# Performance work log

Hardware: AMD Instinct MI355X
Metric: run time of the kernel (lower is better)

The kernel has to match this reference:

```python
import jax, jax.numpy as jnp
import numpy as np

B, N, CPTS = 16, 4096, 64
M, K, RADIUS = 1024, 32, 0.2
MLP = [64, 64, 128]
EPS = 1e-5  # torch BatchNorm2d default


def setup_inputs() -> dict:
    key = jax.random.key(0)
    ks = jax.random.split(key, 2 + len(MLP))
    inp = {
        "xyz": jax.random.uniform(ks[0], (B, N, 3), dtype=jnp.float32),
        "points": jax.random.normal(ks[1], (B, N, CPTS), dtype=jnp.float32),
    }
    cin = 3 + CPTS
    for i, cout in enumerate(MLP):
        inp[f"W{i}"] = jax.random.normal(ks[2 + i], (cout, cin), dtype=jnp.float32) / np.sqrt(cin)
        inp[f"g{i}"] = jnp.ones((cout,), jnp.float32)
        inp[f"b{i}"] = jnp.zeros((cout,), jnp.float32)
        cin = cout
    return inp


def fps(xyz, m):
    # Farthest point sampling, deterministic start at index 0. Returns (B, m) int32.
    b, n, _ = xyz.shape

    def step(carry, _):
        min_d, far = carry
        cent = jnp.take_along_axis(xyz, far[:, None, None], axis=1)  # (B,1,3)
        d = jnp.sum((xyz - cent) ** 2, axis=-1)                      # (B,N)
        min_d = jnp.minimum(min_d, d)
        return (min_d, jnp.argmax(min_d, axis=-1).astype(jnp.int32)), far

    init = (jnp.full((b, n), 1e10, xyz.dtype), jnp.zeros((b,), jnp.int32))
    _, inds = jax.lax.scan(step, init, None, length=m)
    return inds.T  # (B, m)


def ball_query(xyz, new_xyz, radius, k):
    # Euclidean distances (B,M,N); indices within radius, first-k, pad with first valid.
    d2 = (jnp.sum(new_xyz ** 2, -1)[:, :, None] + jnp.sum(xyz ** 2, -1)[:, None, :]
          - 2.0 * jnp.einsum('bmc,bnc->bmn', new_xyz, xyz))
    dists = jnp.sqrt(jnp.maximum(d2, 0.0))
    n = xyz.shape[1]
    idx = jnp.where(dists > radius, n, jnp.arange(n, dtype=jnp.int32)[None, None, :])
    idx = jnp.sort(idx, axis=-1)[:, :, :k]          # first k in-radius indices (N-padded)
    first = idx[:, :, :1]                           # centroid itself (dist 0) always valid
    return jnp.where(idx == n, first, idx)          # (B, M, k)


def reference(xyz, points, W0, g0, b0, W1, g1, b1, W2, g2, b2):
    bidx = jnp.arange(B)[:, None]
    fps_inds = fps(xyz, M)                          # (B, M)
    new_xyz = xyz[bidx, fps_inds]                   # (B, M, 3)
    g_inds = ball_query(xyz, new_xyz, RADIUS, K)    # (B, M, K)
    bidx2 = jnp.arange(B)[:, None, None]
    grouped_xyz = xyz[bidx2, g_inds] - new_xyz[:, :, None, :]   # (B,M,K,3) local coords
    grouped_pts = points[bidx2, g_inds]                          # (B,M,K,C)
    feats = jnp.concatenate([grouped_xyz, grouped_pts], axis=-1)  # (B,M,K,3+C)

    # 1x1 Conv2d (no bias) + BatchNorm2d (training-mode batch stats) + ReLU
    for Wi, gi, bi in ((W0, g0, b0), (W1, g1, b1), (W2, g2, b2)):
        h = jnp.einsum('bmkc,oc->bmko', feats, Wi)
        mean = h.mean(axis=(0, 1, 2))
        var = h.var(axis=(0, 1, 2))
        feats = jax.nn.relu(gi * (h - mean) * jax.lax.rsqrt(var + EPS) + bi)

    new_points = feats.max(axis=2)                  # max-pool over K -> (B, M, 128)
    return new_xyz, new_points, g_inds
```

## Files before the change

### kernel.cpp

```cpp
#include <hip/hip_runtime.h>
#include <hip/hip_bf16.h>
#include <cstdint>

#define B_ 16
#define N_ 4096
#define CPTS_ 64
#define M_ 1024
#define K_ 32
#define MF_TOT 2097152

using ushort8 = __attribute__((ext_vector_type(8))) unsigned short;

static __device__ __forceinline__ unsigned f2bf(float x){
  unsigned u = __float_as_uint(x);
  return (u + 0x7fffu + ((u >> 16) & 1u)) >> 16;
}
static __device__ __forceinline__ float bf2f(unsigned short u){
  return __uint_as_float(((unsigned)u) << 16);
}

#define DPPMAX(v, ctrl)                                                        \
  do {                                                                         \
    int _t = __builtin_amdgcn_update_dpp(0, __float_as_int(v), (ctrl), 0xf,    \
                                         0xf, true);                           \
    (v) = fmaxf((v), __int_as_float(_t));                                      \
  } while (0)

#define STEP(MD, PX, PY, PZ, C, J)                                             \
  { float dx = PX.C - cx, dy = PY.C - cy, dz = PZ.C - cz;                      \
    float d = dx * dx; d = d + dy * dy; d = d + dz * dz;                       \
    float nm = fminf(MD.C, d); MD.C = nm;                                      \
    if (nm > bv){ bv = nm; bj = (J); } }
#define STEP4(MD, PX, PY, PZ, J0)                                              \
  STEP(MD, PX, PY, PZ, x, J0)                                                  \
  STEP(MD, PX, PY, PZ, y, (J0) + 1)                                            \
  STEP(MD, PX, PY, PZ, z, (J0) + 2)                                            \
  STEP(MD, PX, PY, PZ, w, (J0) + 3)

__global__ __launch_bounds__(512, 1) void fps_kernel(const float* __restrict__ xyz,
                                                     float* __restrict__ newxyz){
#pragma clang fp contract(off)
  __shared__ float xs[N_], ys[N_], zs[N_];
  __shared__ int inds_s[M_];
  __shared__ unsigned long long sv_[2][8];
  const int b = blockIdx.x, tid = threadIdx.x;
  const int lane = tid & 63, wv = tid >> 6;
  const float* xb = xyz + (size_t)b * N_ * 3;
  for (int i = tid; i < N_ * 3; i += 512){
    float v = xb[i];
    int n = i / 3, c = i - n * 3;
    if (c == 0) xs[n] = v; else if (c == 1) ys[n] = v; else zs[n] = v;
  }
  __syncthreads();
  const float4 px0 = *reinterpret_cast<const float4*>(&xs[tid * 8 + 0]);
  const float4 px1 = *reinterpret_cast<const float4*>(&xs[tid * 8 + 4]);
  const float4 py0 = *reinterpret_cast<const float4*>(&ys[tid * 8 + 0]);
  const float4 py1 = *reinterpret_cast<const float4*>(&ys[tid * 8 + 4]);
  const float4 pz0 = *reinterpret_cast<const float4*>(&zs[tid * 8 + 0]);
  const float4 pz1 = *reinterpret_cast<const float4*>(&zs[tid * 8 + 4]);
  float4 md0 = make_float4(1e10f, 1e10f, 1e10f, 1e10f);
  float4 md1 = md0;
  int far = 0;
  float cx = xs[0], cy = ys[0], cz = zs[0];
  for (int m = 0; m < M_; ++m){
    if (tid == 0) inds_s[m] = far;
    float bv = -1.0f; int bj = 0;
    STEP4(md0, px0, py0, pz0, 0)
    STEP4(md1, px1, py1, pz1, 4)
    float wm = bv;
    DPPMAX(wm, 0x111);
    DPPMAX(wm, 0x112);
    DPPMAX(wm, 0x114);
    DPPMAX(wm, 0x118);
    DPPMAX(wm, 0x142);
    DPPMAX(wm, 0x143);
    const float wmax = __int_as_float(
        __builtin_amdgcn_readlane(__float_as_int(wm), 63));
    unsigned long long tied = __ballot(bv == wmax);
    const int winlane = (int)__builtin_ctzll(tied);
    const int sl = m & 1;
    if (lane == winlane){
      int wn = tid * 8 + bj;
      sv_[sl][wv] = ((unsigned long long)__float_as_uint(wmax) << 32)
                  | (unsigned)(4095 - wn);
    }
    __syncthreads();
    unsigned long long p0 = sv_[sl][0], p1 = sv_[sl][1], p2 = sv_[sl][2], p3 = sv_[sl][3];
    unsigned long long p4 = sv_[sl][4], p5 = sv_[sl][5], p6 = sv_[sl][6], p7 = sv_[sl][7];
    if (p1 > p0) p0 = p1;
    if (p3 > p2) p2 = p3;
    if (p5 > p4) p4 = p5;
    if (p7 > p6) p6 = p7;
    if (p2 > p0) p0 = p2;
    if (p6 > p4) p4 = p6;
    if (p4 > p0) p0 = p4;
    far = 4095 - (int)(p0 & 0xffffffffu);
    cx = xs[far]; cy = ys[far]; cz = zs[far];
  }
  __syncthreads();
  for (int t = tid; t < M_; t += 512){
    int id = inds_s[t];
    size_t o = ((size_t)b * M_ + t) * 3;
    newxyz[o] = xs[id]; newxyz[o + 1] = ys[id]; newxyz[o + 2] = zs[id];
  }
}

__global__ __launch_bounds__(256) void phi_kernel(const float* __restrict__ xyz,
                                                  const float* __restrict__ points,
                                                  const float* __restrict__ W,
                                                  float* __restrict__ phi){
  __shared__ __align__(16) float Wt[67][64];
  __shared__ __align__(16) float ft[67][128];
  const int tid = threadIdx.x, blk = blockIdx.x;
  const int p0 = blk * 128;
  for (int i = tid; i < 67 * 64; i += 256){
    int o = i / 67, c = i - o * 67;
    Wt[c][o] = W[i];
  }
  const int sl = tid >> 1, half = tid & 1;
  const int p = p0 + sl;
  const float* ps = points + (size_t)p * CPTS_ + half * 32;
  #pragma unroll
  for (int j = 0; j < 8; ++j){
    float4 v = *reinterpret_cast<const float4*>(ps + j * 4);
    int c = 3 + half * 32 + j * 4;
    ft[c][sl] = v.x; ft[c + 1][sl] = v.y; ft[c + 2][sl] = v.z; ft[c + 3][sl] = v.w;
  }
  if (half == 0){
    const float* xp = xyz + (size_t)p * 3;
    ft[0][sl] = xp[0]; ft[1][sl] = xp[1]; ft[2][sl] = xp[2];
  }
  __syncthreads();
  const int sg = tid & 31, og = tid >> 5;
  float acc[4][8];
  #pragma unroll
  for (int i = 0; i < 4; ++i)
    #pragma unroll
    for (int o = 0; o < 8; ++o) acc[i][o] = 0.0f;
  #pragma unroll 2
  for (int c = 0; c < 67; ++c){
    float4 f = *reinterpret_cast<const float4*>(&ft[c][sg * 4]);
    float4 w0 = *reinterpret_cast<const float4*>(&Wt[c][og * 8]);
    float4 w1 = *reinterpret_cast<const float4*>(&Wt[c][og * 8 + 4]);
    const float fv[4] = {f.x, f.y, f.z, f.w};
    #pragma unroll
    for (int i = 0; i < 4; ++i){
      acc[i][0] += fv[i] * w0.x; acc[i][1] += fv[i] * w0.y;
      acc[i][2] += fv[i] * w0.z; acc[i][3] += fv[i] * w0.w;
      acc[i][4] += fv[i] * w1.x; acc[i][5] += fv[i] * w1.y;
      acc[i][6] += fv[i] * w1.z; acc[i][7] += fv[i] * w1.w;
    }
  }
  #pragma unroll
  for (int i = 0; i < 4; ++i){
    float* dst = phi + (size_t)(p0 + sg * 4 + i) * 64 + og * 8;
    *reinterpret_cast<float4*>(dst)     = make_float4(acc[i][0], acc[i][1], acc[i][2], acc[i][3]);
    *reinterpret_cast<float4*>(dst + 4) = make_float4(acc[i][4], acc[i][5], acc[i][6], acc[i][7]);
  }
}

__global__ __launch_bounds__(256) void ballq_psi_kernel(const float* __restrict__ xyz,
                                                        const float* __restrict__ newxyz,
                                                        int* __restrict__ gi,
                                                        float* __restrict__ gif,
                                                        const float* __restrict__ W0,
                                                        float* __restrict__ psi){
  if (blockIdx.x >= 4096){
    const int mi = (blockIdx.x - 4096) * 256 + threadIdx.x;
    const float x = newxyz[(size_t)mi * 3];
    const float y = newxyz[(size_t)mi * 3 + 1];
    const float z = newxyz[(size_t)mi * 3 + 2];
    float* dst = psi + (size_t)mi * 64;
    #pragma unroll
    for (int o4 = 0; o4 < 16; ++o4){
      float v[4];
      #pragma unroll
      for (int e = 0; e < 4; ++e){
        int o = o4 * 4 + e;
        v[e] = fmaf(z, W0[o * 67 + 2], fmaf(y, W0[o * 67 + 1], x * W0[o * 67]));
      }
      *reinterpret_cast<float4*>(dst + o4 * 4) = make_float4(v[0], v[1], v[2], v[3]);
    }
    return;
  }
  const int gw = (blockIdx.x * 256 + threadIdx.x) >> 6;
  const int lane = threadIdx.x & 63;
  const int b = gw >> 10, m = gw & 1023;
  const float* xb = xyz + (size_t)b * N_ * 3;
  const size_t no = (size_t)b * M_ + m;
  const float cx = newxyz[no * 3], cy = newxyz[no * 3 + 1], cz = newxyz[no * 3 + 2];
  const float sm = fmaf(cz, cz, fmaf(cy, cy, cx * cx));
  int total = 0, first_idx = 0; bool havef = false;
  int*   gd = gi  + no * K_;
  float* fd = gif + no * K_;
  for (int ch = 0; ch < 64 && total < K_; ++ch){
    const int n = ch * 64 + lane;
    const float x = xb[n * 3], y = xb[n * 3 + 1], z = xb[n * 3 + 2];
    const float sn = fmaf(z, z, fmaf(y, y, x * x));
    const float dt = fmaf(z, cz, fmaf(y, cy, x * cx));
    float d2 = (sm + sn) - 2.0f * dt;
    float dist = sqrtf(fmaxf(d2, 0.0f));
    bool pred = !(dist > 0.2f);
    unsigned long long mask = __ballot(pred);
    if (!havef && mask){ havef = true; first_idx = ch * 64 + (int)__builtin_ctzll(mask); }
    if (pred){
      int rank = total + (int)__popcll(mask & ((1ull << lane) - 1ull));
      if (rank < K_){ gd[rank] = n; fd[rank] = (float)n; }
    }
    total += (int)__popcll(mask);
  }
  if (total < K_ && lane >= total && lane < K_){ gd[lane] = first_idx; fd[lane] = (float)first_idx; }
}

__global__ __launch_bounds__(256) void stats0_kernel(const float* __restrict__ phi,
                                                     const float* __restrict__ psi,
                                                     const int* __restrict__ gi,
                                                     float* __restrict__ part){
  __shared__ int gidx[128];
  __shared__ float psm[4][64];
  const int tid = threadIdx.x, blk = blockIdx.x;
  const size_t s0 = (size_t)blk * 128;
  const int b  = (int)(s0 >> 15);
  const int m0 = ((int)(s0 & 32767)) >> 5;
  if (tid < 128) gidx[tid] = gi[(size_t)b * 32768 + (size_t)m0 * K_ + tid];
  psm[tid >> 6][tid & 63] =
      psi[((size_t)b * M_ + m0 + (tid >> 6)) * 64 + (tid & 63)];
  __syncthreads();
  const int sg = tid & 31, og = tid >> 5;
  const int mi = sg >> 3;
  float sv[8], sq[8];
  #pragma unroll
  for (int o = 0; o < 8; ++o){ sv[o] = 0.f; sq[o] = 0.f; }
  #pragma unroll
  for (int i = 0; i < 4; ++i){
    const int g = gidx[sg * 4 + i];
    const float* gp = phi + ((size_t)b * N_ + g) * 64 + og * 8;
    float4 a0 = *reinterpret_cast<const float4*>(gp);
    float4 a1 = *reinterpret_cast<const float4*>(gp + 4);
    const float pv[8] = {a0.x, a0.y, a0.z, a0.w, a1.x, a1.y, a1.z, a1.w};
    #pragma unroll
    for (int o = 0; o < 8; ++o){
      float v = pv[o] - psm[mi][og * 8 + o];
      sv[o] += v; sq[o] += v * v;
    }
  }
  #pragma unroll
  for (int off = 1; off < 32; off <<= 1){
    #pragma unroll
    for (int o = 0; o < 8; ++o){
      sv[o] += __shfl_xor(sv[o], off);
      sq[o] += __shfl_xor(sq[o], off);
    }
  }
  if (sg == 0){
    #pragma unroll
    for (int o = 0; o < 8; ++o){
      int ch = og * 8 + o;
      part[(size_t)(ch * 2) * 4096 + blk]     = sv[o];
      part[(size_t)(ch * 2 + 1) * 4096 + blk] = sq[o];
    }
  }
}

template<int CIN, int COUT, int MIN_, int MOUT_>
__global__ __launch_bounds__(256) void mlp_pass(
    const float* __restrict__ phi, const float* __restrict__ psi,
    const int* __restrict__ gi,
    const unsigned short* __restrict__ hin, const float* __restrict__ bnin,
    const float* __restrict__ W,
    unsigned short* __restrict__ hout, float* __restrict__ part,
    float* __restrict__ out)
{
  constexpr int OPT = COUT / 8;
  static_assert(OPT % 4 == 0, "OPT");
  __shared__ __align__(16) float Wt[CIN][COUT];
  __shared__ __align__(16) float ft[CIN][128];
  const int tid = threadIdx.x, blk = blockIdx.x;
  const size_t s0 = (size_t)blk * 128;

  for (int i = tid; i < CIN * COUT; i += 256){
    int o = i / CIN, c = i - o * CIN;
    Wt[c][o] = W[i];
  }

  if constexpr (MIN_ == 3){
    __shared__ int gidx[128];
    __shared__ float psm[4][64];
    const int b  = (int)(s0 >> 15);
    const int m0 = ((int)(s0 & 32767)) >> 5;
    if (tid < 128) gidx[tid] = gi[(size_t)b * 32768 + (size_t)m0 * K_ + tid];
    psm[tid >> 6][tid & 63] =
        psi[((size_t)b * M_ + m0 + (tid >> 6)) * 64 + (tid & 63)];
    __syncthreads();
    const int sl = tid >> 1, half = tid & 1;
    const int g = gidx[sl];
    const int mi = sl >> 5;
    const float* gp = phi + ((size_t)b * N_ + g) * 64 + half * 32;
    #pragma unroll
    for (int j = 0; j < 8; ++j){
      float4 v = *reinterpret_cast<const float4*>(gp + j * 4);
      int c = half * 32 + j * 4;
      ft[c][sl]     = fmaxf((v.x - psm[mi][c])     * bnin[c]     + bnin[CIN + c],     0.0f);
      ft[c + 1][sl] = fmaxf((v.y - psm[mi][c + 1]) * bnin[c + 1] + bnin[CIN + c + 1], 0.0f);
      ft[c + 2][sl] = fmaxf((v.z - psm[mi][c + 2]) * bnin[c + 2] + bnin[CIN + c + 2], 0.0f);
      ft[c + 3][sl] = fmaxf((v.w - psm[mi][c + 3]) * bnin[c + 3] + bnin[CIN + c + 3], 0.0f);
    }
  } else {
    const int sl = tid >> 1, c0 = (tid & 1) * 32;
    const unsigned short* hp = hin + (s0 + sl) * CIN + c0;
    #pragma unroll
    for (int j = 0; j < 4; ++j){
      ushort8 raw = *reinterpret_cast<const ushort8*>(hp + j * 8);
      #pragma unroll
      for (int e = 0; e < 8; ++e){
        int c = c0 + j * 8 + e;
        float h = bf2f(raw[e]);
        float f = h * bnin[c] + bnin[CIN + c];
        ft[c][sl] = fmaxf(f, 0.0f);
      }
    }
  }
  __syncthreads();

  const int sg = tid & 31, og = tid >> 5;
  float acc[4][OPT];
  #pragma unroll
  for (int i = 0; i < 4; ++i)
    #pragma unroll
    for (int o = 0; o < OPT; ++o) acc[i][o] = 0.0f;

  #pragma unroll 2
  for (int c = 0; c < CIN; ++c){
    float4 f = *reinterpret_cast<const float4*>(&ft[c][sg * 4]);
    float4 w[OPT / 4];
    #pragma unroll
    for (int j = 0; j < OPT / 4; ++j)
      w[j] = *reinterpret_cast<const float4*>(&Wt[c][og * OPT + j * 4]);
    const float fv[4] = {f.x, f.y, f.z, f.w};
    #pragma unroll
    for (int i = 0; i < 4; ++i){
      #pragma unroll
      for (int j = 0; j < OPT / 4; ++j){
        acc[i][j * 4 + 0] += fv[i] * w[j].x;
        acc[i][j * 4 + 1] += fv[i] * w[j].y;
        acc[i][j * 4 + 2] += fv[i] * w[j].z;
        acc[i][j * 4 + 3] += fv[i] * w[j].w;
      }
    }
  }

  if constexpr (MOUT_ == 0){
    #pragma unroll
    for (int i = 0; i < 4; ++i){
      size_t s = s0 + sg * 4 + i;
      unsigned pk[OPT / 2];
      #pragma unroll
      for (int o = 0; o < OPT / 2; ++o)
        pk[o] = f2bf(acc[i][2 * o]) | (f2bf(acc[i][2 * o + 1]) << 16);
      uint4* dst = reinterpret_cast<uint4*>(hout + s * COUT + og * OPT);
      dst[0] = make_uint4(pk[0], pk[1], pk[2], pk[3]);
      if constexpr (OPT == 16) dst[1] = make_uint4(pk[4], pk[5], pk[6], pk[7]);
    }
  }
  {
    float sv[OPT], sq[OPT];
    #pragma unroll
    for (int o = 0; o < OPT; ++o){
      float a0 = acc[0][o], a1 = acc[1][o], a2 = acc[2][o], a3 = acc[3][o];
      sv[o] = ((a0 + a1) + a2) + a3;
      sq[o] = ((a0 * a0 + a1 * a1) + a2 * a2) + a3 * a3;
    }
    #pragma unroll
    for (int off = 1; off < 32; off <<= 1){
      #pragma unroll
      for (int o = 0; o < OPT; ++o){
        sv[o] += __shfl_xor(sv[o], off);
        sq[o] += __shfl_xor(sq[o], off);
      }
    }
    if (sg == 0){
      #pragma unroll
      for (int o = 0; o < OPT; ++o){
        int ch = og * OPT + o;
        part[(size_t)(ch * 2) * 4096 + blk]     = sv[o];
        part[(size_t)(ch * 2 + 1) * 4096 + blk] = sq[o];
      }
    }
  }
  if constexpr (MOUT_ == 4){
    float amx[OPT], amn[OPT];
    #pragma unroll
    for (int o = 0; o < OPT; ++o){
      amx[o] = fmaxf(fmaxf(acc[0][o], acc[1][o]), fmaxf(acc[2][o], acc[3][o]));
      amn[o] = fminf(fminf(acc[0][o], acc[1][o]), fminf(acc[2][o], acc[3][o]));
    }
    #pragma unroll
    for (int off = 1; off < 8; off <<= 1){
      #pragma unroll
      for (int o = 0; o < OPT; ++o){
        amx[o] = fmaxf(amx[o], __shfl_xor(amx[o], off));
        amn[o] = fminf(amn[o], __shfl_xor(amn[o], off));
      }
    }
    if ((sg & 7) == 0){
      size_t mf = (s0 >> 5) + (sg >> 3);
      float* dmx = out + mf * COUT + og * OPT;
      float* dmn = dmx + MF_TOT;
      #pragma unroll
      for (int j = 0; j < OPT / 4; ++j){
        *reinterpret_cast<float4*>(dmx + j * 4) =
            make_float4(amx[j * 4], amx[j * 4 + 1], amx[j * 4 + 2], amx[j * 4 + 3]);
        *reinterpret_cast<float4*>(dmn + j * 4) =
            make_float4(amn[j * 4], amn[j * 4 + 1], amn[j * 4 + 2], amn[j * 4 + 3]);
      }
    }
  }
}

__global__ __launch_bounds__(256) void reduce_stats(const float* __restrict__ part,
                                                    const float* __restrict__ g,
                                                    const float* __restrict__ bb,
                                                    float* __restrict__ bn, int cout){
  const int ch = blockIdx.x, tid = threadIdx.x;
  float s = 0.f, q = 0.f;
  const float* ps = part + (size_t)(ch * 2) * 4096;
  const float* pq = part + (size_t)(ch * 2 + 1) * 4096;
  for (int i = tid; i < 4096; i += 256){ s += ps[i]; q += pq[i]; }
  #pragma unroll
  for (int off = 1; off < 64; off <<= 1){ s += __shfl_xor(s, off); q += __shfl_xor(q, off); }
  __shared__ float as_[4], aq_[4];
  if ((tid & 63) == 0){ as_[tid >> 6] = s; aq_[tid >> 6] = q; }
  __syncthreads();
  if (tid == 0){
    float S = as_[0] + as_[1] + as_[2] + as_[3];
    float Q = aq_[0] + aq_[1] + aq_[2] + aq_[3];
    const float cnt = 524288.0f;
    float mean = S / cnt;
    float var  = Q / cnt - mean * mean;
    float sc = g[ch] / sqrtf(var + 1e-5f);
    bn[ch] = sc;
    bn[cout + ch] = bb[ch] - mean * sc;
  }
}

__global__ __launch_bounds__(256) void bn_minmax_finish(const float* __restrict__ mxmn,
                                                        const float* __restrict__ bn2,
                                                        float* __restrict__ out){
  const int i = blockIdx.x * 256 + threadIdx.x;
  const int ch = i & 127;
  const float a = bn2[ch], sh = bn2[128 + ch];
  const float mx = mxmn[i], mn = mxmn[MF_TOT + i];
  out[i] = fmaxf(fmaxf(mx * a + sh, mn * a + sh), 0.0f);
}

extern "C" void kernel_launch(void* const* d_in, const int* in_sizes, int n_in,
                              void* d_out, int out_size, void* d_ws, size_t ws_size,
                              hipStream_t stream){
  (void)in_sizes; (void)n_in; (void)out_size; (void)ws_size;
  const float* xyz    = (const float*)d_in[0];
  const float* points = (const float*)d_in[1];
  const float* W0 = (const float*)d_in[2];
  const float* g0 = (const float*)d_in[3];
  const float* b0 = (const float*)d_in[4];
  const float* W1 = (const float*)d_in[5];
  const float* g1 = (const float*)d_in[6];
  const float* b1 = (const float*)d_in[7];
  const float* W2 = (const float*)d_in[8];
  const float* g2 = (const float*)d_in[9];
  const float* b2 = (const float*)d_in[10];

  float* out = (float*)d_out;
  float* o_newxyz = out;
  float* o_newpts = out + (size_t)B_ * M_ * 3;
  float* o_gind   = out + (size_t)B_ * M_ * 3 + (size_t)B_ * M_ * 128;

  char* ws = (char*)d_ws;
  int*   gi   = (int*)(ws + 0);
  float* part = (float*)(ws + (2ull << 20));
  float* bn0  = (float*)(ws + (6ull << 20));
  float* bn1  = (float*)(ws + (6ull << 20) + 1024);
  float* bn2  = (float*)(ws + (6ull << 20) + 2048);
  float* phi  = (float*)(ws + (8ull << 20));
  float* psi  = (float*)(ws + (24ull << 20));
  unsigned short* h1 = (unsigned short*)(ws + (28ull << 20));
  float* mxmn = (float*)(ws + (92ull << 20));

  phi_kernel<<<512, 256, 0, stream>>>(xyz, points, W0, phi);
  fps_kernel<<<16, 512, 0, stream>>>(xyz, o_newxyz);
  ballq_psi_kernel<<<4160, 256, 0, stream>>>(xyz, o_newxyz, gi, o_gind, W0, psi);

  stats0_kernel<<<4096, 256, 0, stream>>>(phi, psi, gi, part);
  reduce_stats<<<64, 256, 0, stream>>>(part, g0, b0, bn0, 64);

  mlp_pass<64, 64, 3, 0><<<4096, 256, 0, stream>>>(phi, psi, gi,
      nullptr, bn0, W1, h1, part, nullptr);
  reduce_stats<<<64, 256, 0, stream>>>(part, g1, b1, bn1, 64);

  mlp_pass<64, 128, 1, 4><<<4096, 256, 0, stream>>>(nullptr, nullptr, nullptr,
      h1, bn1, W2, nullptr, part, mxmn);
  reduce_stats<<<128, 256, 0, stream>>>(part, g2, b2, bn2, 128);
  bn_minmax_finish<<<MF_TOT / 256, 256, 0, stream>>>(mxmn, bn2, o_newpts);
}
```

Baseline: 1.048 ms.

## Run third MLP layer on bf16 MFMA with split hi/lo precision

The 64->128 layer moves off the scalar FP32 FMA loop and onto MFMA 16x16x32 bf16 instructions. Activations and weights are each split into a bf16 high part and a bf16 residual, and three MFMAs per product recover near-FP32 accuracy. The kernel's epilogue now takes BN statistics and per-group max/min directly from the MFMA accumulator layout. The original template is specialised into a layer-1-only kernel. The cost is three MFMAs per tile and more LDS for the split operands, and accuracy is slightly below true FP32.

```diff
diff --git a/kernel.cpp b/kernel.cpp
--- a/kernel.cpp
+++ b/kernel.cpp
@@ -10,6 +10,8 @@
 #define MF_TOT 2097152
 
 using ushort8 = __attribute__((ext_vector_type(8))) unsigned short;
+using bf16x8  = __attribute__((ext_vector_type(8))) short;
+using f32x4v  = __attribute__((ext_vector_type(4))) float;
 
 static __device__ __forceinline__ unsigned f2bf(float x){
   unsigned u = __float_as_uint(x);
@@ -262,17 +264,14 @@
   }
 }
 
-template<int CIN, int COUT, int MIN_, int MOUT_>
-__global__ __launch_bounds__(256) void mlp_pass(
+template<int CIN, int COUT>
+__global__ __launch_bounds__(256) void mlp1_pass(
     const float* __restrict__ phi, const float* __restrict__ psi,
-    const int* __restrict__ gi,
-    const unsigned short* __restrict__ hin, const float* __restrict__ bnin,
+    const int* __restrict__ gi, const float* __restrict__ bnin,
     const float* __restrict__ W,
-    unsigned short* __restrict__ hout, float* __restrict__ part,
-    float* __restrict__ out)
+    unsigned short* __restrict__ hout, float* __restrict__ part)
 {
   constexpr int OPT = COUT / 8;
-  static_assert(OPT % 4 == 0, "OPT");
   __shared__ __align__(16) float Wt[CIN][COUT];
   __shared__ __align__(16) float ft[CIN][128];
   const int tid = threadIdx.x, blk = blockIdx.x;
@@ -282,8 +281,7 @@
     int o = i / CIN, c = i - o * CIN;
     Wt[c][o] = W[i];
   }
-
-  if constexpr (MIN_ == 3){
+  {
     __shared__ int gidx[128];
     __shared__ float psm[4][64];
     const int b  = (int)(s0 >> 15);
@@ -305,20 +303,6 @@
       ft[c + 2][sl] = fmaxf((v.z - psm[mi][c + 2]) * bnin[c + 2] + bnin[CIN + c + 2], 0.0f);
       ft[c + 3][sl] = fmaxf((v.w - psm[mi][c + 3]) * bnin[c + 3] + bnin[CIN + c + 3], 0.0f);
     }
-  } else {
-    const int sl = tid >> 1, c0 = (tid & 1) * 32;
-    const unsigned short* hp = hin + (s0 + sl) * CIN + c0;
-    #pragma unroll
-    for (int j = 0; j < 4; ++j){
-      ushort8 raw = *reinterpret_cast<const ushort8*>(hp + j * 8);
-      #pragma unroll
-      for (int e = 0; e < 8; ++e){
-        int c = c0 + j * 8 + e;
-        float h = bf2f(raw[e]);
-        float f = h * bnin[c] + bnin[CIN + c];
-        ft[c][sl] = fmaxf(f, 0.0f);
-      }
-    }
   }
   __syncthreads();
 
@@ -349,69 +333,156 @@
     }
   }
 
-  if constexpr (MOUT_ == 0){
-    #pragma unroll
-    for (int i = 0; i < 4; ++i){
-      size_t s = s0 + sg * 4 + i;
-      unsigned pk[OPT / 2];
+  #pragma unroll
+  for (int i = 0; i < 4; ++i){
+    size_t s = s0 + sg * 4 + i;
+    unsigned pk[OPT / 2];
+    #pragma unroll
+    for (int o = 0; o < OPT / 2; ++o)
+      pk[o] = f2bf(acc[i][2 * o]) | (f2bf(acc[i][2 * o + 1]) << 16);
+    uint4* dst = reinterpret_cast<uint4*>(hout + s * COUT + og * OPT);
+    dst[0] = make_uint4(pk[0], pk[1], pk[2], pk[3]);
+  }
+  float sv[OPT], sq[OPT];
+  #pragma unroll
+  for (int o = 0; o < OPT; ++o){
+    float a0 = acc[0][o], a1 = acc[1][o], a2 = acc[2][o], a3 = acc[3][o];
+    sv[o] = ((a0 + a1) + a2) + a3;
+    sq[o] = ((a0 * a0 + a1 * a1) + a2 * a2) + a3 * a3;
+  }
+  #pragma unroll
+  for (int off = 1; off < 32; off <<= 1){
+    #pragma unroll
+    for (int o = 0; o < OPT; ++o){
+      sv[o] += __shfl_xor(sv[o], off);
+      sq[o] += __shfl_xor(sq[o], off);
+    }
+  }
+  if (sg == 0){
+    #pragma unroll
+    for (int o = 0; o < OPT; ++o){
+      int ch = og * OPT + o;
+      part[(size_t)(ch * 2) * 4096 + blk]     = sv[o];
+      part[(size_t)(ch * 2 + 1) * 4096 + blk] = sq[o];
+    }
+  }
+}
+
+__global__ __launch_bounds__(256) void mlp2_mfma(
+    const unsigned short* __restrict__ h1, const float* __restrict__ bn1,
+    const float* __restrict__ W2, float* __restrict__ part,
+    float* __restrict__ mxmn)
+{
+  __shared__ unsigned short wsh[128 * 72], wsl[128 * 72];
+  __shared__ unsigned short fsh[128 * 72], fsl[128 * 72];
+  const int tid = threadIdx.x, blk = blockIdx.x;
+  const size_t s0 = (size_t)blk * 128;
+
+  for (int i = tid; i < 128 * 64; i += 256){
+    int o = i >> 6, c = i & 63;
+    float f = W2[i];
+    unsigned hb = f2bf(f);
+    float res = f - bf2f((unsigned short)hb);
+    wsh[o * 72 + c] = (unsigned short)hb;
+    wsl[o * 72 + c] = (unsigned short)f2bf(res);
+  }
+  {
+    const int sl = tid >> 1, c0 = (tid & 1) * 32;
+    const unsigned short* hp = h1 + (s0 + sl) * 64 + c0;
+    #pragma unroll
+    for (int j = 0; j < 4; ++j){
+      ushort8 raw = *reinterpret_cast<const ushort8*>(hp + j * 8);
+      ushort8 ph, pl;
       #pragma unroll
-      for (int o = 0; o < OPT / 2; ++o)
-        pk[o] = f2bf(acc[i][2 * o]) | (f2bf(acc[i][2 * o + 1]) << 16);
-      uint4* dst = reinterpret_cast<uint4*>(hout + s * COUT + og * OPT);
-      dst[0] = make_uint4(pk[0], pk[1], pk[2], pk[3]);
-      if constexpr (OPT == 16) dst[1] = make_uint4(pk[4], pk[5], pk[6], pk[7]);
-    }
-  }
-  {
-    float sv[OPT], sq[OPT];
-    #pragma unroll
-    for (int o = 0; o < OPT; ++o){
-      float a0 = acc[0][o], a1 = acc[1][o], a2 = acc[2][o], a3 = acc[3][o];
-      sv[o] = ((a0 + a1) + a2) + a3;
-      sq[o] = ((a0 * a0 + a1 * a1) + a2 * a2) + a3 * a3;
-    }
-    #pragma unroll
-    for (int off = 1; off < 32; off <<= 1){
+      for (int e = 0; e < 8; ++e){
+        int c = c0 + j * 8 + e;
+        float f = fmaxf(bf2f(raw[e]) * bn1[c] + bn1[64 + c], 0.0f);
+        unsigned hb = f2bf(f);
+        float res = f - bf2f((unsigned short)hb);
+        ph[e] = (unsigned short)hb;
+        pl[e] = (unsigned short)f2bf(res);
+      }
+      *reinterpret_cast<ushort8*>(&fsh[sl * 72 + c0 + j * 8]) = ph;
+      *reinterpret_cast<ushort8*>(&fsl[sl * 72 + c0 + j * 8]) = pl;
+    }
+  }
+  __syncthreads();
+
+  const int l = tid & 63, w = tid >> 6;
+  const int col = l & 15, g = l >> 4;
+
+  bf16x8 bh[2][2], bl[2][2];
+  #pragma unroll
+  for (int ot = 0; ot < 2; ++ot)
+    #pragma unroll
+    for (int ks = 0; ks < 2; ++ks){
+      int a = (w * 32 + ot * 16 + col) * 72 + ks * 32 + g * 8;
+      bh[ot][ks] = *reinterpret_cast<const bf16x8*>(&wsh[a]);
+      bl[ot][ks] = *reinterpret_cast<const bf16x8*>(&wsl[a]);
+    }
+
+  f32x4v acc[8][2];
+  #pragma unroll
+  for (int st = 0; st < 8; ++st)
+    #pragma unroll
+    for (int ot = 0; ot < 2; ++ot)
+      acc[st][ot] = (f32x4v){0.f, 0.f, 0.f, 0.f};
+
+  #pragma unroll
+  for (int st = 0; st < 8; ++st){
+    bf16x8 ah[2], al[2];
+    #pragma unroll
+    for (int ks = 0; ks < 2; ++ks){
+      int a = (st * 16 + col) * 72 + ks * 32 + g * 8;
+      ah[ks] = *reinterpret_cast<const bf16x8*>(&fsh[a]);
+      al[ks] = *reinterpret_cast<const bf16x8*>(&fsl[a]);
+    }
+    #pragma unroll
+    for (int ot = 0; ot < 2; ++ot){
       #pragma unroll
-      for (int o = 0; o < OPT; ++o){
-        sv[o] += __shfl_xor(sv[o], off);
-        sq[o] += __shfl_xor(sq[o], off);
+      for (int ks = 0; ks < 2; ++ks){
+        acc[st][ot] = __builtin_amdgcn_mfma_f32_16x16x32_bf16(ah[ks], bh[ot][ks], acc[st][ot], 0, 0, 0);
+        acc[st][ot] = __builtin_amdgcn_mfma_f32_16x16x32_bf16(ah[ks], bl[ot][ks], acc[st][ot], 0, 0, 0);
+        acc[st][ot] = __builtin_amdgcn_mfma_f32_16x16x32_bf16(al[ks], bh[ot][ks], acc[st][ot], 0, 0, 0);
       }
     }
-    if (sg == 0){
+  }
+
+  #pragma unroll
+  for (int ot = 0; ot < 2; ++ot){
+    const int ch = w * 32 + ot * 16 + col;
+    float sv = 0.f, sq = 0.f;
+    float mxm[4], mnm[4];
+    #pragma unroll
+    for (int j = 0; j < 4; ++j){ mxm[j] = -1e30f; mnm[j] = 1e30f; }
+    #pragma unroll
+    for (int st = 0; st < 8; ++st){
+      f32x4v a = acc[st][ot];
+      float t0 = a[0], t1 = a[1], t2 = a[2], t3 = a[3];
+      sv += ((t0 + t1) + t2) + t3;
+      sq += ((t0 * t0 + t1 * t1) + t2 * t2) + t3 * t3;
+      float tmx = fmaxf(fmaxf(t0, t1), fmaxf(t2, t3));
+      float tmn = fminf(fminf(t0, t1), fminf(t2, t3));
+      mxm[st >> 1] = fmaxf(mxm[st >> 1], tmx);
+      mnm[st >> 1] = fminf(mnm[st >> 1], tmn);
+    }
+    sv += __shfl_xor(sv, 16); sv += __shfl_xor(sv, 32);
+    sq += __shfl_xor(sq, 16); sq += __shfl_xor(sq, 32);
+    #pragma unroll
+    for (int j = 0; j < 4; ++j){
+      mxm[j] = fmaxf(mxm[j], __shfl_xor(mxm[j], 16));
+      mxm[j] = fmaxf(mxm[j], __shfl_xor(mxm[j], 32));
+      mnm[j] = fminf(mnm[j], __shfl_xor(mnm[j], 16));
+      mnm[j] = fminf(mnm[j], __shfl_xor(mnm[j], 32));
+    }
+    if (g == 0){
+      part[(size_t)(ch * 2) * 4096 + blk]     = sv;
+      part[(size_t)(ch * 2 + 1) * 4096 + blk] = sq;
       #pragma unroll
-      for (int o = 0; o < OPT; ++o){
-        int ch = og * OPT + o;
-        part[(size_t)(ch * 2) * 4096 + blk]     = sv[o];
-        part[(size_t)(ch * 2 + 1) * 4096 + blk] = sq[o];
-      }
-    }
-  }
-  if constexpr (MOUT_ == 4){
-    float amx[OPT], amn[OPT];
-    #pragma unroll
-    for (int o = 0; o < OPT; ++o){
-      amx[o] = fmaxf(fmaxf(acc[0][o], acc[1][o]), fmaxf(acc[2][o], acc[3][o]));
-      amn[o] = fminf(fminf(acc[0][o], acc[1][o]), fminf(acc[2][o], acc[3][o]));
-    }
-    #pragma unroll
-    for (int off = 1; off < 8; off <<= 1){
-      #pragma unroll
-      for (int o = 0; o < OPT; ++o){
-        amx[o] = fmaxf(amx[o], __shfl_xor(amx[o], off));
-        amn[o] = fminf(amn[o], __shfl_xor(amn[o], off));
-      }
-    }
-    if ((sg & 7) == 0){
-      size_t mf = (s0 >> 5) + (sg >> 3);
-      float* dmx = out + mf * COUT + og * OPT;
-      float* dmn = dmx + MF_TOT;
-      #pragma unroll
-      for (int j = 0; j < OPT / 4; ++j){
-        *reinterpret_cast<float4*>(dmx + j * 4) =
-            make_float4(amx[j * 4], amx[j * 4 + 1], amx[j * 4 + 2], amx[j * 4 + 3]);
-        *reinterpret_cast<float4*>(dmn + j * 4) =
-            make_float4(amn[j * 4], amn[j * 4 + 1], amn[j * 4 + 2], amn[j * 4 + 3]);
+      for (int j = 0; j < 4; ++j){
+        size_t mf = (s0 >> 5) + j;
+        mxmn[mf * 128 + ch]          = mxm[j];
+        mxmn[MF_TOT + mf * 128 + ch] = mnm[j];
       }
     }
   }
@@ -492,12 +563,10 @@
   stats0_kernel<<<4096, 256, 0, stream>>>(phi, psi, gi, part);
   reduce_stats<<<64, 256, 0, stream>>>(part, g0, b0, bn0, 64);
 
-  mlp_pass<64, 64, 3, 0><<<4096, 256, 0, stream>>>(phi, psi, gi,
-      nullptr, bn0, W1, h1, part, nullptr);
+  mlp1_pass<64, 64><<<4096, 256, 0, stream>>>(phi, psi, gi, bn0, W1, h1, part);
   reduce_stats<<<64, 256, 0, stream>>>(part, g1, b1, bn1, 64);
 
-  mlp_pass<64, 128, 1, 4><<<4096, 256, 0, stream>>>(nullptr, nullptr, nullptr,
-      h1, bn1, W2, nullptr, part, mxmn);
+  mlp2_mfma<<<4096, 256, 0, stream>>>(h1, bn1, W2, part, mxmn);
   reduce_stats<<<128, 256, 0, stream>>>(part, g2, b2, bn2, 128);
   bn_minmax_finish<<<MF_TOT / 256, 256, 0, stream>>>(mxmn, bn2, o_newpts);
 }
```

Measured after the change: 938.0 us. 10.5% less time.
